# Kernel optimization log

Measured on AMD Instinct MI355X. Metric: run time of the kernel, lower is better.

The kernel has to match this reference:

```python
import jax, jax.numpy as jnp
import numpy as np

DIM = 512
HEADS = 8
EPS = 1e-3  # keras LayerNormalization default epsilon


def setup_inputs() -> dict:
    key = jax.random.key(0)
    ks = jax.random.split(key, 12)
    B, H, W, C = 8, 32, 32, DIM
    s = 0.02
    return {
        "x": jax.random.normal(ks[0], (B, H, W, C), jnp.float32),
        "ln_gamma": jnp.ones((C,), jnp.float32),
        "ln_beta": jnp.zeros((C,), jnp.float32),
        "qkv_d_w": jax.random.normal(ks[1], (C, 3 * C), jnp.float32) * s,
        "qkv_d_b": jnp.zeros((3 * C,), jnp.float32),
        "qkv_s_w": jax.random.normal(ks[2], (C, 3 * C), jnp.float32) * s,
        "qkv_s_b": jnp.zeros((3 * C,), jnp.float32),
        "proj_d_w": jax.random.normal(ks[3], (C, C), jnp.float32) * s,
        "proj_d_b": jnp.zeros((C,), jnp.float32),
        "proj_s_w": jax.random.normal(ks[4], (C, C), jnp.float32) * s,
        "proj_s_b": jnp.zeros((C,), jnp.float32),
        "fusion_weight": jnp.ones((2,), jnp.float32),
    }


def _split_heads(t, B, N):
    # [B, N, C] -> [B, heads, N, head_dim]
    return t.reshape(B, N, HEADS, -1).transpose(0, 2, 1, 3)


def _merge_heads(t, B, N, C):
    # [B, heads, N, head_dim] -> [B, N, C]
    return t.transpose(0, 2, 1, 3).reshape(B, N, C)


def reference(x, ln_gamma, ln_beta, qkv_d_w, qkv_d_b, qkv_s_w, qkv_s_b,
              proj_d_w, proj_d_b, proj_s_w, proj_s_b, fusion_weight):
    B, H, W, C = x.shape
    N = H * W
    scale = (C // HEADS) ** -0.5

    xf = x.reshape(B, N, C)
    mu = jnp.mean(xf, axis=-1, keepdims=True)
    var = jnp.var(xf, axis=-1, keepdims=True)
    xf = (xf - mu) * jax.lax.rsqrt(var + EPS) * ln_gamma + ln_beta

    # dense (softmax) branch
    qkv_d = xf @ qkv_d_w + qkv_d_b
    q_d, k_d, v_d = (
        _split_heads(t, B, N) for t in jnp.split(qkv_d, 3, axis=-1)
    )
    logits_d = jnp.einsum("bhnd,bhmd->bhnm", q_d, k_d) * scale
    out_d = jnp.einsum("bhnm,bhmd->bhnd", jax.nn.softmax(logits_d, axis=-1), v_d)
    out_d = _merge_heads(out_d, B, N, C) @ proj_d_w + proj_d_b

    # sparse (relu^2) branch
    qkv_s = xf @ qkv_s_w + qkv_s_b
    q_s, k_s, v_s = (
        _split_heads(t, B, N) for t in jnp.split(qkv_s, 3, axis=-1)
    )
    rq = jnp.square(jax.nn.relu(q_s))
    rk = jnp.square(jax.nn.relu(k_s))
    logits_s = jnp.einsum("bhnd,bhmd->bhnm", rq, rk) * scale
    out_s = jnp.einsum("bhnm,bhmd->bhnd", logits_s, v_s)
    out_s = _merge_heads(out_s, B, N, C) @ proj_s_w + proj_s_b

    alpha = jax.nn.softmax(fusion_weight)
    out = alpha[0] * out_s + alpha[1] * out_d
    return out.reshape(B, H, W, C)
```

## Files before the change

### kernel.cpp

```cpp
#include <hip/hip_runtime.h>
#include <math.h>

#define M_ROWS   8192
#define CDIM     512
#define QKV_N    1536
#define NTOK     1024
#define HEADS    8
#define HD       64
#define EPS      1e-3f
#define SCALE    0.125f
#define SCL2E    0.18033688011112042f

typedef __attribute__((ext_vector_type(8))) short short8;
typedef __attribute__((ext_vector_type(4))) float f32x4;
typedef unsigned short ushort_t;


__device__ __forceinline__ ushort_t f2bf(float f) {
    union { float f; unsigned int u; } v; v.f = f;
    unsigned int r = v.u + 0x7fffu + ((v.u >> 16) & 1u);
    return (ushort_t)(r >> 16);
}
__device__ __forceinline__ float bf2f(ushort_t u) {
    union { unsigned int u; float f; } v; v.u = ((unsigned int)u) << 16;
    return v.f;
}

__device__ __forceinline__ void stage16(const void* g, void* l) {
    __builtin_amdgcn_global_load_lds(
        (__attribute__((address_space(1))) void*)(g),
        (__attribute__((address_space(3))) void*)(l), 16, 0, 0);
}

__device__ __forceinline__ void get_alpha(const float* __restrict__ fw,
                                          float& a0, float& a1)
{
    const float m  = fmaxf(fw[0], fw[1]);
    const float e0 = __expf(fw[0] - m);
    const float e1 = __expf(fw[1] - m);
    const float inv = 1.0f / (e0 + e1);
    a0 = e0 * inv;
    a1 = e1 * inv;
}


__device__ __forceinline__ void tconv_body(const float* __restrict__ W,
                                           ushort_t* __restrict__ hiT,
                                           ushort_t* __restrict__ loT,
                                           int N, int ors, int coff,
                                           int bk, int bn, int t,
                                           float (*tile)[65])
{
#pragma unroll
    for (int i = 0; i < 4; ++i) {
        const int idx = t + i * 256;
        const int kl = idx >> 4, nl = (idx & 15) * 4;
        const float4 v = *(const float4*)(W + (size_t)(bk + kl) * N + bn + nl);
        tile[kl][nl] = v.x; tile[kl][nl + 1] = v.y;
        tile[kl][nl + 2] = v.z; tile[kl][nl + 3] = v.w;
    }
    __syncthreads();
#pragma unroll
    for (int i = 0; i < 2; ++i) {
        const int idx = t + i * 256;
        const int nl = idx >> 3, kc = (idx & 7) * 8;
        short8 hv, lv;
#pragma unroll
        for (int j = 0; j < 8; ++j) {
            const float f = tile[kc + j][nl];
            const ushort_t h = f2bf(f);
            hv[j] = (short)h;
            lv[j] = (short)f2bf(f - bf2f(h));
        }
        const size_t ob = (size_t)(bn + nl) * ors + coff + bk + kc;
        *(short8*)(hiT + ob) = hv;
        if (loT) *(short8*)(loT + ob) = lv;
    }
}

__global__ __launch_bounds__(256) void prep_kernel(const float* __restrict__ x,
                                                   const float* __restrict__ gamma,
                                                   const float* __restrict__ beta,
                                                   ushort_t* __restrict__ xhi,
                                                   ushort_t* __restrict__ xlo,
                                                   const float* __restrict__ qkv_d_w,
                                                   ushort_t* __restrict__ WdT_hi,
                                                   const float* __restrict__ qkv_s_w,
                                                   ushort_t* __restrict__ WsT_hi,
                                                   ushort_t* __restrict__ WsT_lo,
                                                   const float* __restrict__ proj_s_w,
                                                   const float* __restrict__ proj_d_w,
                                                   ushort_t* __restrict__ WpT_hi,
                                                   ushort_t* __restrict__ WpT_lo,
                                                   const float* __restrict__ bs,
                                                   const float* __restrict__ bd,
                                                   const float* __restrict__ fw,
                                                   float* __restrict__ biasc)
{
    __shared__ float tile[64][65];
    const int t = threadIdx.x;
    const int blk = blockIdx.x;

    if (blk < 2048) {
        const int wv   = t >> 6, lane = t & 63;
        const int row  = blk * 4 + wv;
        const float* xr = x + (size_t)row * CDIM + lane * 8;
        const float4 v0 = *(const float4*)(xr);
        const float4 v1 = *(const float4*)(xr + 4);
        float s  = (v0.x + v0.y) + (v0.z + v0.w) + (v1.x + v1.y) + (v1.z + v1.w);
        float ss = (v0.x * v0.x + v0.y * v0.y) + (v0.z * v0.z + v0.w * v0.w)
                 + (v1.x * v1.x + v1.y * v1.y) + (v1.z * v1.z + v1.w * v1.w);
#pragma unroll
        for (int off = 32; off > 0; off >>= 1) {
            s  += __shfl_xor(s,  off, 64);
            ss += __shfl_xor(ss, off, 64);
        }
        const float mu  = s * (1.0f / CDIM);
        const float var = ss * (1.0f / CDIM) - mu * mu;
        const float rs  = rsqrtf(var + EPS);
        const float4 g0 = *(const float4*)(gamma + lane * 8);
        const float4 g1 = *(const float4*)(gamma + lane * 8 + 4);
        const float4 b0 = *(const float4*)(beta + lane * 8);
        const float4 b1 = *(const float4*)(beta + lane * 8 + 4);
        float o[8];
        o[0] = (v0.x - mu) * rs * g0.x + b0.x;
        o[1] = (v0.y - mu) * rs * g0.y + b0.y;
        o[2] = (v0.z - mu) * rs * g0.z + b0.z;
        o[3] = (v0.w - mu) * rs * g0.w + b0.w;
        o[4] = (v1.x - mu) * rs * g1.x + b1.x;
        o[5] = (v1.y - mu) * rs * g1.y + b1.y;
        o[6] = (v1.z - mu) * rs * g1.z + b1.z;
        o[7] = (v1.w - mu) * rs * g1.w + b1.w;
        short8 hv, lv;
#pragma unroll
        for (int j = 0; j < 8; ++j) {
            const ushort_t h = f2bf(o[j]);
            hv[j] = (short)h;
            lv[j] = (short)f2bf(o[j] - bf2f(h));
        }
        *(short8*)(xhi + (size_t)row * CDIM + lane * 8) = hv;
        *(short8*)(xlo + (size_t)row * CDIM + lane * 8) = lv;
        return;
    }
    int idx = blk - 2048;
    if (idx < 192) {
        tconv_body(qkv_d_w, WdT_hi, nullptr, QKV_N, CDIM, 0,
                   (idx & 7) * 64, (idx >> 3) * 64, t, tile);
        return;
    }
    idx -= 192;
    if (idx < 192) {
        tconv_body(qkv_s_w, WsT_hi, WsT_lo, QKV_N, CDIM, 0,
                   (idx & 7) * 64, (idx >> 3) * 64, t, tile);
        return;
    }
    idx -= 192;
    if (idx < 64) {
        tconv_body(proj_s_w, WpT_hi, WpT_lo, CDIM, 1024, 0,
                   (idx & 7) * 64, (idx >> 3) * 64, t, tile);
        return;
    }
    idx -= 64;
    if (idx < 64) {
        tconv_body(proj_d_w, WpT_hi, nullptr, CDIM, 1024, 512,
                   (idx & 7) * 64, (idx >> 3) * 64, t, tile);
        return;
    }
    float a0, a1;
    get_alpha(fw, a0, a1);
    biasc[t]       = a0 * bs[t]       + a1 * bd[t];
    biasc[t + 256] = a0 * bs[t + 256] + a1 * bd[t + 256];
}


template<int MODE, int OUTBF>
__global__ __launch_bounds__(256) void gemm_bf16_mfma(const ushort_t* __restrict__ Ahi,
                                                      const ushort_t* __restrict__ Alo,
                                                      const ushort_t* __restrict__ Bhi,
                                                      const ushort_t* __restrict__ Blo,
                                                      const float* __restrict__ bias,
                                                      float* __restrict__ C,
                                                      ushort_t* __restrict__ Cb,
                                                      int N, int K)
{
    const int t  = threadIdx.x;
    const int l  = t & 63, w = t >> 6;
    const int wr = w >> 1, wc = w & 1;
    const int lr = l & 15, lg = l >> 4;
    const int bm = blockIdx.x * 128, bn = blockIdx.y * 128;

    __shared__ ushort_t As[MODE ? 2 : 1][128 * 64];
    __shared__ ushort_t Bs[MODE ? 2 : 1][128 * 64];

    f32x4 acc[4][4];
#pragma unroll
    for (int i = 0; i < 4; ++i)
#pragma unroll
        for (int j = 0; j < 4; ++j) acc[i][j] = (f32x4){0.f, 0.f, 0.f, 0.f};

    const int srow8 = t >> 3;
    const int sch   = ((t & 7) ^ ((t >> 3) & 7)) * 8;
    const int lbase = (t >> 6) * 512;

    for (int kt = 0; kt < K; kt += 64) {
        __syncthreads();
#pragma unroll
        for (int i = 0; i < 4; ++i) {
            const int row = srow8 + i * 32;
            const size_t ga = (size_t)(bm + row) * K + kt + sch;
            const size_t gb = (size_t)(bn + row) * K + kt + sch;
            stage16(Ahi + ga, &As[0][i * 2048 + lbase]);
            stage16(Bhi + gb, &Bs[0][i * 2048 + lbase]);
            if (MODE) {
                stage16(Alo + ga, &As[MODE ? 1 : 0][i * 2048 + lbase]);
                stage16(Blo + gb, &Bs[MODE ? 1 : 0][i * 2048 + lbase]);
            }
        }
        __syncthreads();
#pragma unroll
        for (int ks = 0; ks < 2; ++ks) {
            short8 ah[4], bh[4], al[4], bl[4];
#pragma unroll
            for (int mf = 0; mf < 4; ++mf) {
                const int row = wr * 64 + mf * 16 + lr;
                const int cs  = (((ks * 4 + lg) ^ (row & 7)) * 8);
                ah[mf] = *(const short8*)(&As[0][row * 64 + cs]);
                if (MODE) al[mf] = *(const short8*)(&As[MODE ? 1 : 0][row * 64 + cs]);
            }
#pragma unroll
            for (int nf = 0; nf < 4; ++nf) {
                const int row = wc * 64 + nf * 16 + lr;
                const int cs  = (((ks * 4 + lg) ^ (row & 7)) * 8);
                bh[nf] = *(const short8*)(&Bs[0][row * 64 + cs]);
                if (MODE) bl[nf] = *(const short8*)(&Bs[MODE ? 1 : 0][row * 64 + cs]);
            }
#pragma unroll
            for (int mf = 0; mf < 4; ++mf)
#pragma unroll
                for (int nf = 0; nf < 4; ++nf) {
                    acc[mf][nf] = __builtin_amdgcn_mfma_f32_16x16x32_bf16(ah[mf], bh[nf], acc[mf][nf], 0, 0, 0);
                    if (MODE) {
                        acc[mf][nf] = __builtin_amdgcn_mfma_f32_16x16x32_bf16(al[mf], bh[nf], acc[mf][nf], 0, 0, 0);
                        acc[mf][nf] = __builtin_amdgcn_mfma_f32_16x16x32_bf16(ah[mf], bl[nf], acc[mf][nf], 0, 0, 0);
                    }
                }
        }
    }
    float bv[4];
#pragma unroll
    for (int nf = 0; nf < 4; ++nf) bv[nf] = bias[bn + wc * 64 + nf * 16 + lr];
    const float oscl = (OUTBF && bn < 512) ? SCL2E : 1.0f;
#pragma unroll
    for (int mf = 0; mf < 4; ++mf)
#pragma unroll
        for (int r = 0; r < 4; ++r) {
            const int row = bm + wr * 64 + mf * 16 + lg * 4 + r;
            if (OUTBF) {
                ushort_t* cp = Cb + (size_t)row * N + bn + wc * 64;
#pragma unroll
                for (int nf = 0; nf < 4; ++nf)
                    cp[nf * 16 + lr] = f2bf((acc[mf][nf][r] + bv[nf]) * oscl);
            } else {
                float* cp = C + (size_t)row * N + bn + wc * 64;
#pragma unroll
                for (int nf = 0; nf < 4; ++nf)
                    cp[nf * 16 + lr] = acc[mf][nf][r] + bv[nf];
            }
        }
}


__global__ __launch_bounds__(256) void gemm_proj(const ushort_t* __restrict__ Ahi,
                                                 const ushort_t* __restrict__ Alo,
                                                 const ushort_t* __restrict__ Bhi,
                                                 const ushort_t* __restrict__ Blo,
                                                 const float* __restrict__ bias,
                                                 float* __restrict__ C)
{
    const int t  = threadIdx.x;
    const int l  = t & 63, w = t >> 6;
    const int wr = w >> 1, wc = w & 1;
    const int lr = l & 15, lg = l >> 4;
    const int bm = blockIdx.x * 64, bn = blockIdx.y * 128;

    __shared__ ushort_t As[2][64 * 64];
    __shared__ ushort_t Bs[2][128 * 64];

    f32x4 acc[2][4];
#pragma unroll
    for (int i = 0; i < 2; ++i)
#pragma unroll
        for (int j = 0; j < 4; ++j) acc[i][j] = (f32x4){0.f, 0.f, 0.f, 0.f};

    const int srow8 = t >> 3;
    const int sch   = ((t & 7) ^ ((t >> 3) & 7)) * 8;
    const int lbase = (t >> 6) * 512;

    for (int kt = 0; kt < 512; kt += 64) {
        __syncthreads();
#pragma unroll
        for (int i = 0; i < 2; ++i) {
            const size_t ga = (size_t)(bm + srow8 + i * 32) * 1024 + kt + sch;
            stage16(Ahi + ga, &As[0][i * 2048 + lbase]);
            stage16(Alo + ga, &As[1][i * 2048 + lbase]);
        }
#pragma unroll
        for (int i = 0; i < 4; ++i) {
            const size_t gb = (size_t)(bn + srow8 + i * 32) * 1024 + kt + sch;
            stage16(Bhi + gb, &Bs[0][i * 2048 + lbase]);
            stage16(Blo + gb, &Bs[1][i * 2048 + lbase]);
        }
        __syncthreads();
#pragma unroll
        for (int ks = 0; ks < 2; ++ks) {
            short8 ah[2], al[2], bh[4], bl[4];
#pragma unroll
            for (int mf = 0; mf < 2; ++mf) {
                const int row = wr * 32 + mf * 16 + lr;
                const int cs  = (((ks * 4 + lg) ^ (row & 7)) * 8);
                ah[mf] = *(const short8*)(&As[0][row * 64 + cs]);
                al[mf] = *(const short8*)(&As[1][row * 64 + cs]);
            }
#pragma unroll
            for (int nf = 0; nf < 4; ++nf) {
                const int row = wc * 64 + nf * 16 + lr;
                const int cs  = (((ks * 4 + lg) ^ (row & 7)) * 8);
                bh[nf] = *(const short8*)(&Bs[0][row * 64 + cs]);
                bl[nf] = *(const short8*)(&Bs[1][row * 64 + cs]);
            }
#pragma unroll
            for (int mf = 0; mf < 2; ++mf)
#pragma unroll
                for (int nf = 0; nf < 4; ++nf) {
                    acc[mf][nf] = __builtin_amdgcn_mfma_f32_16x16x32_bf16(ah[mf], bh[nf], acc[mf][nf], 0, 0, 0);
                    acc[mf][nf] = __builtin_amdgcn_mfma_f32_16x16x32_bf16(al[mf], bh[nf], acc[mf][nf], 0, 0, 0);
                    acc[mf][nf] = __builtin_amdgcn_mfma_f32_16x16x32_bf16(ah[mf], bl[nf], acc[mf][nf], 0, 0, 0);
                }
        }
    }

    for (int kt = 512; kt < 1024; kt += 64) {
        __syncthreads();
#pragma unroll
        for (int i = 0; i < 2; ++i) {
            const size_t ga = (size_t)(bm + srow8 + i * 32) * 1024 + kt + sch;
            stage16(Ahi + ga, &As[0][i * 2048 + lbase]);
        }
#pragma unroll
        for (int i = 0; i < 4; ++i) {
            const size_t gb = (size_t)(bn + srow8 + i * 32) * 1024 + kt + sch;
            stage16(Bhi + gb, &Bs[0][i * 2048 + lbase]);
        }
        __syncthreads();
#pragma unroll
        for (int ks = 0; ks < 2; ++ks) {
            short8 ah[2], bh[4];
#pragma unroll
            for (int mf = 0; mf < 2; ++mf) {
                const int row = wr * 32 + mf * 16 + lr;
                const int cs  = (((ks * 4 + lg) ^ (row & 7)) * 8);
                ah[mf] = *(const short8*)(&As[0][row * 64 + cs]);
            }
#pragma unroll
            for (int nf = 0; nf < 4; ++nf) {
                const int row = wc * 64 + nf * 16 + lr;
                const int cs  = (((ks * 4 + lg) ^ (row & 7)) * 8);
                bh[nf] = *(const short8*)(&Bs[0][row * 64 + cs]);
            }
#pragma unroll
            for (int mf = 0; mf < 2; ++mf)
#pragma unroll
                for (int nf = 0; nf < 4; ++nf)
                    acc[mf][nf] = __builtin_amdgcn_mfma_f32_16x16x32_bf16(ah[mf], bh[nf], acc[mf][nf], 0, 0, 0);
        }
    }

    float bv[4];
#pragma unroll
    for (int nf = 0; nf < 4; ++nf) bv[nf] = bias[bn + wc * 64 + nf * 16 + lr];
#pragma unroll
    for (int mf = 0; mf < 2; ++mf)
#pragma unroll
        for (int r = 0; r < 4; ++r) {
            const int row = bm + wr * 32 + mf * 16 + lg * 4 + r;
            float* cp = C + (size_t)row * CDIM + bn + wc * 64;
#pragma unroll
            for (int nf = 0; nf < 4; ++nf)
                cp[nf * 16 + lr] = acc[mf][nf][r] + bv[nf];
        }
}


__global__ __launch_bounds__(256) void vt_skv_kernel(const ushort_t* __restrict__ qkvd_bf,
                                                     ushort_t* __restrict__ vtg,
                                                     const float* __restrict__ qkvs,
                                                     float* __restrict__ kvpart)
{
    __shared__ __align__(16) float smem[8704];
    const int t = threadIdx.x;

    if (blockIdx.x < 1024) {
        ushort_t* tile = (ushort_t*)smem;
        const int bh = blockIdx.x & 63, nt = blockIdx.x >> 6;
        const int b  = bh >> 3, h = bh & 7;
        const int row = t >> 2, c16 = (t & 3) * 16;
        const size_t src = (size_t)(b * NTOK + nt * 64 + row) * QKV_N + 2 * CDIM + h * HD + c16;
        *(short8*)(tile + row * 72 + c16)     = *(const short8*)(qkvd_bf + src);
        *(short8*)(tile + row * 72 + c16 + 8) = *(const short8*)(qkvd_bf + src + 8);
        __syncthreads();
        const int d = t >> 2, tc = (t & 3) * 16;
        short8 o0, o1;
#pragma unroll
        for (int i = 0; i < 8; ++i) {
            o0[i] = (short)tile[(tc + i) * 72 + d];
            o1[i] = (short)tile[(tc + 8 + i) * 72 + d];
        }
        const size_t dst = ((size_t)bh * 64 + d) * NTOK + nt * 64 + tc;
        *(short8*)(vtg + dst)     = o0;
        *(short8*)(vtg + dst + 8) = o1;
        return;
    }

    const int bid   = blockIdx.x - 1024;
    const int bh    = bid >> 2;
    const int chunk = bid & 3;
    const int b     = bh >> 3, h = bh & 7;
    const int j     = t >> 2, g = t & 3;
    float* ks = smem;
    float* vs = smem + 64 * 68;
    float4 acc[4];
#pragma unroll
    for (int c4 = 0; c4 < 4; ++c4) acc[c4] = make_float4(0.f, 0.f, 0.f, 0.f);

    const size_t bbase = (size_t)b * NTOK * QKV_N;
    for (int mt = chunk * 4; mt < chunk * 4 + 4; ++mt) {
        __syncthreads();
        {
            const float* ksrc = qkvs + bbase + (size_t)(mt * 64) * QKV_N + CDIM + h * HD;
            const float* vsrc = ksrc + CDIM;
#pragma unroll
            for (int i = 0; i < 4; ++i) {
                const int idx = t + i * 256;
                const int row = idx >> 4, c4 = (idx & 15) * 4;
                *(float4*)(ks + row * 68 + c4) = *(const float4*)(ksrc + (size_t)row * QKV_N + c4);
                *(float4*)(vs + row * 68 + c4) = *(const float4*)(vsrc + (size_t)row * QKV_N + c4);
            }
        }
        __syncthreads();
#pragma unroll 4
        for (int m = 0; m < 64; ++m) {
            const float kkv = ks[m * 68 + j];
            const float rk  = fmaxf(kkv, 0.f);
            const float rk2 = rk * rk;
#pragma unroll
            for (int c4 = 0; c4 < 4; ++c4) {
                const float4 vv = *(const float4*)(vs + m * 68 + g * 16 + c4 * 4);
                acc[c4].x += rk2 * vv.x; acc[c4].y += rk2 * vv.y;
                acc[c4].z += rk2 * vv.z; acc[c4].w += rk2 * vv.w;
            }
        }
    }
#pragma unroll
    for (int c4 = 0; c4 < 4; ++c4) {
        float4 w = acc[c4];
        w.x *= SCALE; w.y *= SCALE; w.z *= SCALE; w.w *= SCALE;
        *(float4*)(kvpart + ((size_t)bid << 12) + j * 64 + g * 16 + c4 * 4) = w;
    }
}


__global__ __launch_bounds__(256) void attn_sout_kernel(const ushort_t* __restrict__ qkvd_bf,
                                                        const ushort_t* __restrict__ vtg,
                                                        const float* __restrict__ qkvs,
                                                        const float* __restrict__ kvpart,
                                                        const float* __restrict__ fw,
                                                        ushort_t* __restrict__ athi,
                                                        ushort_t* __restrict__ atlo)
{
    __shared__ __align__(16) float smem[9216];
    const int t = threadIdx.x;

    if (blockIdx.x < 1024) {
        const int l  = t & 63;
        const int w  = t >> 6;
        const int lr = l & 15;
        const int lg = l >> 4;

        const int blk = blockIdx.x;
        const int xcd = blk & 7;
        const int ixl = blk >> 3;
        const int bh  = ((ixl >> 4) << 3) + xcd;
        const int qt  = ixl & 15;
        const int b   = bh >> 3, h = bh & 7;

        ushort_t* Qs = (ushort_t*)smem;
        ushort_t* Ks = Qs + 64 * 72;
        ushort_t* Vs = Ks + 64 * 72;
        ushort_t* Pq = Vs + 64 * 72;

        const int srow = t >> 2, sc = (t & 3) * 16;
        const size_t kbase = (size_t)(b * NTOK + srow) * QKV_N + CDIM + h * HD + sc;
        const size_t vbase = ((size_t)bh * 64 + srow) * NTOK + sc;

        {
            const size_t src = (size_t)(b * NTOK + qt * 64 + srow) * QKV_N + h * HD + sc;
            *(short8*)(Qs + srow * 72 + sc)     = *(const short8*)(qkvd_bf + src);
            *(short8*)(Qs + srow * 72 + sc + 8) = *(const short8*)(qkvd_bf + src + 8);
        }

        short8 kr0 = *(const short8*)(qkvd_bf + kbase);
        short8 kr1 = *(const short8*)(qkvd_bf + kbase + 8);
        short8 vr0 = *(const short8*)(vtg + vbase);
        short8 vr1 = *(const short8*)(vtg + vbase + 8);

        __syncthreads();

        const short8 bQ0 = *(const short8*)(Qs + (w * 16 + lr) * 72 + lg * 8);
        const short8 bQ1 = *(const short8*)(Qs + (w * 16 + lr) * 72 + 32 + lg * 8);

        f32x4 oacc[4];
#pragma unroll
        for (int i = 0; i < 4; ++i) oacc[i] = (f32x4){0.f, 0.f, 0.f, 0.f};
        float lsum = 0.f;

        for (int kt2 = 0; kt2 < 16; ++kt2) {
            *(short8*)(Ks + srow * 72 + sc)     = kr0;
            *(short8*)(Ks + srow * 72 + sc + 8) = kr1;
            *(short8*)(Vs + srow * 72 + sc)     = vr0;
            *(short8*)(Vs + srow * 72 + sc + 8) = vr1;
            __syncthreads();

            if (kt2 < 15) {
                const size_t ksrc = kbase + (size_t)((kt2 + 1) * 64) * QKV_N;
                const size_t vsrc = vbase + (kt2 + 1) * 64;
                kr0 = *(const short8*)(qkvd_bf + ksrc);
                kr1 = *(const short8*)(qkvd_bf + ksrc + 8);
                vr0 = *(const short8*)(vtg + vsrc);
                vr1 = *(const short8*)(vtg + vsrc + 8);
            }

#pragma unroll
            for (int kb = 0; kb < 4; ++kb) {
                const short8 aK0 = *(const short8*)(Ks + (kb * 16 + lr) * 72 + lg * 8);
                const short8 aK1 = *(const short8*)(Ks + (kb * 16 + lr) * 72 + 32 + lg * 8);
                f32x4 z = {0.f, 0.f, 0.f, 0.f};
                __builtin_amdgcn_s_setprio(1);
                z = __builtin_amdgcn_mfma_f32_16x16x32_bf16(aK0, bQ0, z, 0, 0, 0);
                z = __builtin_amdgcn_mfma_f32_16x16x32_bf16(aK1, bQ1, z, 0, 0, 0);
                __builtin_amdgcn_s_setprio(0);
                const float p0 = exp2f(z[0]);
                const float p1 = exp2f(z[1]);
                const float p2 = exp2f(z[2]);
                const float p3 = exp2f(z[3]);
                lsum += (p0 + p1) + (p2 + p3);
                unsigned int r01, r23;
                asm("v_cvt_pk_bf16_f32 %0, %1, %2" : "=v"(r01) : "v"(p0), "v"(p1));
                asm("v_cvt_pk_bf16_f32 %0, %1, %2" : "=v"(r23) : "v"(p2), "v"(p3));
                uint2 pw; pw.x = r01; pw.y = r23;
                *(uint2*)(Pq + (w * 16 + lr) * 72 + kb * 16 + lg * 4) = pw;
            }

            const short8 bP0 = *(const short8*)(Pq + (w * 16 + lr) * 72 + lg * 8);
            const short8 bP1 = *(const short8*)(Pq + (w * 16 + lr) * 72 + 32 + lg * 8);
            __builtin_amdgcn_s_setprio(1);
#pragma unroll
            for (int nfd = 0; nfd < 4; ++nfd) {
                const short8 aV0 = *(const short8*)(Vs + (nfd * 16 + lr) * 72 + lg * 8);
                const short8 aV1 = *(const short8*)(Vs + (nfd * 16 + lr) * 72 + 32 + lg * 8);
                oacc[nfd] = __builtin_amdgcn_mfma_f32_16x16x32_bf16(aV0, bP0, oacc[nfd], 0, 0, 0);
                oacc[nfd] = __builtin_amdgcn_mfma_f32_16x16x32_bf16(aV1, bP1, oacc[nfd], 0, 0, 0);
            }
            __builtin_amdgcn_s_setprio(0);
            __syncthreads();
        }

        lsum += __shfl_xor(lsum, 16, 64);
        lsum += __shfl_xor(lsum, 32, 64);
        float a0, a1;
        get_alpha(fw, a0, a1);
        const float sc2 = a1 / lsum;
        const size_t orow = ((size_t)(b * NTOK + qt * 64 + w * 16 + lr)) * 1024 + CDIM + h * HD;
#pragma unroll
        for (int nfd = 0; nfd < 4; ++nfd) {
            ushort4 hw;
#pragma unroll
            for (int r = 0; r < 4; ++r)
                ((ushort_t*)&hw)[r] = f2bf(oacc[nfd][r] * sc2);
            *(ushort4*)(athi + orow + nfd * 16 + lg * 4) = hw;
        }
        return;
    }

    const int blk = blockIdx.x - 1024;
    const int qt  = blk & 15;
    const int bh  = blk >> 4;
    const int b   = bh >> 3, h = bh & 7;
    const int r   = t >> 2, g = t & 3;
    float* qs  = smem;
    float* kvs = smem + 64 * 68;
    {
        const float* qsrc = qkvs + (size_t)b * NTOK * QKV_N + (size_t)(qt * 64) * QKV_N + h * HD;
        const float* p0 = kvpart + ((size_t)(bh * 4) << 12);
#pragma unroll
        for (int i = 0; i < 4; ++i) {
            const int idx = t + i * 256;
            const int row = idx >> 4, c4 = (idx & 15) * 4;
            *(float4*)(qs + row * 68 + c4) = *(const float4*)(qsrc + (size_t)row * QKV_N + c4);
            const int o = row * 64 + c4;
            float4 s0 = *(const float4*)(p0 + o);
            const float4 s1 = *(const float4*)(p0 + 4096 + o);
            const float4 s2 = *(const float4*)(p0 + 8192 + o);
            const float4 s3 = *(const float4*)(p0 + 12288 + o);
            s0.x += s1.x + s2.x + s3.x; s0.y += s1.y + s2.y + s3.y;
            s0.z += s1.z + s2.z + s3.z; s0.w += s1.w + s2.w + s3.w;
            *(float4*)(kvs + row * 68 + c4) = s0;
        }
    }
    __syncthreads();
    float4 acc[4];
#pragma unroll
    for (int c4 = 0; c4 < 4; ++c4) acc[c4] = make_float4(0.f, 0.f, 0.f, 0.f);
#pragma unroll 4
    for (int jj = 0; jj < 64; ++jj) {
        const float qv  = qs[r * 68 + jj];
        const float rq  = fmaxf(qv, 0.f);
        const float rq2 = rq * rq;
#pragma unroll
        for (int c4 = 0; c4 < 4; ++c4) {
            const float4 kvv = *(const float4*)(kvs + jj * 68 + g * 16 + c4 * 4);
            acc[c4].x += rq2 * kvv.x; acc[c4].y += rq2 * kvv.y;
            acc[c4].z += rq2 * kvv.z; acc[c4].w += rq2 * kvv.w;
        }
    }
    float a0, a1;
    get_alpha(fw, a0, a1);
    const size_t orow = ((size_t)(b * NTOK + qt * 64 + r)) * 1024 + h * HD;
#pragma unroll
    for (int c4 = 0; c4 < 4; ++c4) {
        float4 w = acc[c4];
        w.x *= a0; w.y *= a0; w.z *= a0; w.w *= a0;
        ushort4 hw, lw;
        hw.x = f2bf(w.x); lw.x = f2bf(w.x - bf2f(hw.x));
        hw.y = f2bf(w.y); lw.y = f2bf(w.y - bf2f(hw.y));
        hw.z = f2bf(w.z); lw.z = f2bf(w.z - bf2f(hw.z));
        hw.w = f2bf(w.w); lw.w = f2bf(w.w - bf2f(hw.w));
        *(ushort4*)(athi + orow + g * 16 + c4 * 4) = hw;
        *(ushort4*)(atlo + orow + g * 16 + c4 * 4) = lw;
    }
}


extern "C" void kernel_launch(void* const* d_in, const int* in_sizes, int n_in,
                              void* d_out, int out_size, void* d_ws, size_t ws_size,
                              hipStream_t stream)
{
    (void)in_sizes; (void)n_in; (void)out_size; (void)ws_size;

    const float* x        = (const float*)d_in[0];
    const float* ln_g     = (const float*)d_in[1];
    const float* ln_b     = (const float*)d_in[2];
    const float* qkv_d_w  = (const float*)d_in[3];
    const float* qkv_d_b  = (const float*)d_in[4];
    const float* qkv_s_w  = (const float*)d_in[5];
    const float* qkv_s_b  = (const float*)d_in[6];
    const float* proj_d_w = (const float*)d_in[7];
    const float* proj_d_b = (const float*)d_in[8];
    const float* proj_s_w = (const float*)d_in[9];
    const float* proj_s_b = (const float*)d_in[10];
    const float* fw       = (const float*)d_in[11];

    float* ws = (float*)d_ws;
    float*    qkvs    = ws;
    float*    kvpart  = ws + (size_t)12582912;
    float*    biasc   = ws + (size_t)13631488;
    ushort_t* qkvd_bf = (ushort_t*)(ws + (size_t)14680064);
    ushort_t* vtg     = (ushort_t*)(ws + (size_t)20971520);
    ushort_t* athi    = (ushort_t*)(ws + (size_t)23068672);
    ushort_t* atlo    = (ushort_t*)(ws + (size_t)27262976);
    ushort_t* xhi     = (ushort_t*)(ws + (size_t)31457280);
    ushort_t* xlo     = (ushort_t*)(ws + (size_t)33554432);
    ushort_t* WdT_hi  = (ushort_t*)(ws + (size_t)35651584);
    ushort_t* WsT_hi  = (ushort_t*)(ws + (size_t)36044800);
    ushort_t* WsT_lo  = (ushort_t*)(ws + (size_t)36438016);
    ushort_t* WpT_hi  = (ushort_t*)(ws + (size_t)36831232);
    ushort_t* WpT_lo  = (ushort_t*)(ws + (size_t)37093376);

    prep_kernel<<<2561, 256, 0, stream>>>(x, ln_g, ln_b, xhi, xlo,
                                          qkv_d_w, WdT_hi,
                                          qkv_s_w, WsT_hi, WsT_lo,
                                          proj_s_w, proj_d_w, WpT_hi, WpT_lo,
                                          proj_s_b, proj_d_b, fw, biasc);

    gemm_bf16_mfma<0, 1><<<dim3(64, 12), 256, 0, stream>>>(xhi, nullptr, WdT_hi, nullptr,
                                                           qkv_d_b, nullptr, qkvd_bf,
                                                           QKV_N, CDIM);
    gemm_bf16_mfma<1, 0><<<dim3(64, 12), 256, 0, stream>>>(xhi, xlo, WsT_hi, WsT_lo,
                                                           qkv_s_b, qkvs, nullptr,
                                                           QKV_N, CDIM);

    vt_skv_kernel<<<1280, 256, 0, stream>>>(qkvd_bf, vtg, qkvs, kvpart);
    attn_sout_kernel<<<2048, 256, 0, stream>>>(qkvd_bf, vtg, qkvs, kvpart, fw, athi, atlo);

    gemm_proj<<<dim3(128, 4), 256, 0, stream>>>(athi, atlo, WpT_hi, WpT_lo,
                                                biasc, (float*)d_out);
}
```

Before: 176.6 us.

## Process two query tiles per attention block to reuse staged K/V tiles

Each dense-attention block now handles 128 query rows (two 64-row halves) instead of 64, so every K/V tile staged in shared memory serves twice as many queries. The dense part of the grid drops from 1024 to 512 blocks, halving global K/V traffic and the staging and barrier overhead per query. In exchange each thread holds twice the accumulators and Q fragments, which raises register pressure and can lower occupancy, and there are fewer blocks to spread across the GPU.

```diff
diff --git a/kernel.cpp b/kernel.cpp
--- a/kernel.cpp
+++ b/kernel.cpp
@@ -480,7 +480,7 @@
     __shared__ __align__(16) float smem[9216];
     const int t = threadIdx.x;
 
-    if (blockIdx.x < 1024) {
+    if (blockIdx.x < 512) {
         const int l  = t & 63;
         const int w  = t >> 6;
         const int lr = l & 15;
@@ -489,8 +489,8 @@
         const int blk = blockIdx.x;
         const int xcd = blk & 7;
         const int ixl = blk >> 3;
-        const int bh  = ((ixl >> 4) << 3) + xcd;
-        const int qt  = ixl & 15;
+        const int bh  = ((ixl >> 3) << 3) + xcd;
+        const int qt  = ixl & 7;
         const int b   = bh >> 3, h = bh & 7;
 
         ushort_t* Qs = (ushort_t*)smem;
@@ -502,10 +502,16 @@
         const size_t kbase = (size_t)(b * NTOK + srow) * QKV_N + CDIM + h * HD + sc;
         const size_t vbase = ((size_t)bh * 64 + srow) * NTOK + sc;
 
-        {
-            const size_t src = (size_t)(b * NTOK + qt * 64 + srow) * QKV_N + h * HD + sc;
+        short8 bQ0[2], bQ1[2];
+#pragma unroll
+        for (int qh = 0; qh < 2; ++qh) {
+            const size_t src = (size_t)(b * NTOK + qt * 128 + qh * 64 + srow) * QKV_N + h * HD + sc;
             *(short8*)(Qs + srow * 72 + sc)     = *(const short8*)(qkvd_bf + src);
             *(short8*)(Qs + srow * 72 + sc + 8) = *(const short8*)(qkvd_bf + src + 8);
+            __syncthreads();
+            bQ0[qh] = *(const short8*)(Qs + (w * 16 + lr) * 72 + lg * 8);
+            bQ1[qh] = *(const short8*)(Qs + (w * 16 + lr) * 72 + 32 + lg * 8);
+            __syncthreads();
         }
 
         short8 kr0 = *(const short8*)(qkvd_bf + kbase);
@@ -513,15 +519,12 @@
         short8 vr0 = *(const short8*)(vtg + vbase);
         short8 vr1 = *(const short8*)(vtg + vbase + 8);
 
-        __syncthreads();
-
-        const short8 bQ0 = *(const short8*)(Qs + (w * 16 + lr) * 72 + lg * 8);
-        const short8 bQ1 = *(const short8*)(Qs + (w * 16 + lr) * 72 + 32 + lg * 8);
-
-        f32x4 oacc[4];
-#pragma unroll
-        for (int i = 0; i < 4; ++i) oacc[i] = (f32x4){0.f, 0.f, 0.f, 0.f};
-        float lsum = 0.f;
+        f32x4 oacc[2][4];
+#pragma unroll
+        for (int qh = 0; qh < 2; ++qh)
+#pragma unroll
+            for (int i = 0; i < 4; ++i) oacc[qh][i] = (f32x4){0.f, 0.f, 0.f, 0.f};
+        float lsum[2] = {0.f, 0.f};
 
         for (int kt2 = 0; kt2 < 16; ++kt2) {
             *(short8*)(Ks + srow * 72 + sc)     = kr0;
@@ -540,58 +543,64 @@
             }
 
 #pragma unroll
-            for (int kb = 0; kb < 4; ++kb) {
-                const short8 aK0 = *(const short8*)(Ks + (kb * 16 + lr) * 72 + lg * 8);
-                const short8 aK1 = *(const short8*)(Ks + (kb * 16 + lr) * 72 + 32 + lg * 8);
-                f32x4 z = {0.f, 0.f, 0.f, 0.f};
+            for (int qh = 0; qh < 2; ++qh) {
+#pragma unroll
+                for (int kb = 0; kb < 4; ++kb) {
+                    const short8 aK0 = *(const short8*)(Ks + (kb * 16 + lr) * 72 + lg * 8);
+                    const short8 aK1 = *(const short8*)(Ks + (kb * 16 + lr) * 72 + 32 + lg * 8);
+                    f32x4 z = {0.f, 0.f, 0.f, 0.f};
+                    __builtin_amdgcn_s_setprio(1);
+                    z = __builtin_amdgcn_mfma_f32_16x16x32_bf16(aK0, bQ0[qh], z, 0, 0, 0);
+                    z = __builtin_amdgcn_mfma_f32_16x16x32_bf16(aK1, bQ1[qh], z, 0, 0, 0);
+                    __builtin_amdgcn_s_setprio(0);
+                    const float p0 = exp2f(z[0]);
+                    const float p1 = exp2f(z[1]);
+                    const float p2 = exp2f(z[2]);
+                    const float p3 = exp2f(z[3]);
+                    lsum[qh] += (p0 + p1) + (p2 + p3);
+                    unsigned int r01, r23;
+                    asm("v_cvt_pk_bf16_f32 %0, %1, %2" : "=v"(r01) : "v"(p0), "v"(p1));
+                    asm("v_cvt_pk_bf16_f32 %0, %1, %2" : "=v"(r23) : "v"(p2), "v"(p3));
+                    uint2 pw; pw.x = r01; pw.y = r23;
+                    *(uint2*)(Pq + (w * 16 + lr) * 72 + kb * 16 + lg * 4) = pw;
+                }
+                const short8 bP0 = *(const short8*)(Pq + (w * 16 + lr) * 72 + lg * 8);
+                const short8 bP1 = *(const short8*)(Pq + (w * 16 + lr) * 72 + 32 + lg * 8);
                 __builtin_amdgcn_s_setprio(1);
-                z = __builtin_amdgcn_mfma_f32_16x16x32_bf16(aK0, bQ0, z, 0, 0, 0);
-                z = __builtin_amdgcn_mfma_f32_16x16x32_bf16(aK1, bQ1, z, 0, 0, 0);
+#pragma unroll
+                for (int nfd = 0; nfd < 4; ++nfd) {
+                    const short8 aV0 = *(const short8*)(Vs + (nfd * 16 + lr) * 72 + lg * 8);
+                    const short8 aV1 = *(const short8*)(Vs + (nfd * 16 + lr) * 72 + 32 + lg * 8);
+                    oacc[qh][nfd] = __builtin_amdgcn_mfma_f32_16x16x32_bf16(aV0, bP0, oacc[qh][nfd], 0, 0, 0);
+                    oacc[qh][nfd] = __builtin_amdgcn_mfma_f32_16x16x32_bf16(aV1, bP1, oacc[qh][nfd], 0, 0, 0);
+                }
                 __builtin_amdgcn_s_setprio(0);
-                const float p0 = exp2f(z[0]);
-                const float p1 = exp2f(z[1]);
-                const float p2 = exp2f(z[2]);
-                const float p3 = exp2f(z[3]);
-                lsum += (p0 + p1) + (p2 + p3);
-                unsigned int r01, r23;
-                asm("v_cvt_pk_bf16_f32 %0, %1, %2" : "=v"(r01) : "v"(p0), "v"(p1));
-                asm("v_cvt_pk_bf16_f32 %0, %1, %2" : "=v"(r23) : "v"(p2), "v"(p3));
-                uint2 pw; pw.x = r01; pw.y = r23;
-                *(uint2*)(Pq + (w * 16 + lr) * 72 + kb * 16 + lg * 4) = pw;
-            }
-
-            const short8 bP0 = *(const short8*)(Pq + (w * 16 + lr) * 72 + lg * 8);
-            const short8 bP1 = *(const short8*)(Pq + (w * 16 + lr) * 72 + 32 + lg * 8);
-            __builtin_amdgcn_s_setprio(1);
-#pragma unroll
-            for (int nfd = 0; nfd < 4; ++nfd) {
-                const short8 aV0 = *(const short8*)(Vs + (nfd * 16 + lr) * 72 + lg * 8);
-                const short8 aV1 = *(const short8*)(Vs + (nfd * 16 + lr) * 72 + 32 + lg * 8);
-                oacc[nfd] = __builtin_amdgcn_mfma_f32_16x16x32_bf16(aV0, bP0, oacc[nfd], 0, 0, 0);
-                oacc[nfd] = __builtin_amdgcn_mfma_f32_16x16x32_bf16(aV1, bP1, oacc[nfd], 0, 0, 0);
-            }
-            __builtin_amdgcn_s_setprio(0);
+            }
             __syncthreads();
         }
 
-        lsum += __shfl_xor(lsum, 16, 64);
-        lsum += __shfl_xor(lsum, 32, 64);
         float a0, a1;
         get_alpha(fw, a0, a1);
-        const float sc2 = a1 / lsum;
-        const size_t orow = ((size_t)(b * NTOK + qt * 64 + w * 16 + lr)) * 1024 + CDIM + h * HD;
-#pragma unroll
-        for (int nfd = 0; nfd < 4; ++nfd) {
-            ushort4 hw;
-#pragma unroll
-            for (int r = 0; r < 4; ++r)
-                ((ushort_t*)&hw)[r] = f2bf(oacc[nfd][r] * sc2);
-            *(ushort4*)(athi + orow + nfd * 16 + lg * 4) = hw;
+#pragma unroll
+        for (int qh = 0; qh < 2; ++qh) {
+            float ls = lsum[qh];
+            ls += __shfl_xor(ls, 16, 64);
+            ls += __shfl_xor(ls, 32, 64);
+            const float sc2 = a1 / ls;
+            const size_t orow = ((size_t)(b * NTOK + qt * 128 + qh * 64 + w * 16 + lr)) * 1024 + CDIM + h * HD;
+#pragma unroll
+            for (int nfd = 0; nfd < 4; ++nfd) {
+                ushort4 hw;
+#pragma unroll
+                for (int r = 0; r < 4; ++r)
+                    ((ushort_t*)&hw)[r] = f2bf(oacc[qh][nfd][r] * sc2);
+                *(ushort4*)(athi + orow + nfd * 16 + lg * 4) = hw;
+            }
         }
         return;
     }
 
-    const int blk = blockIdx.x - 1024;
+    const int blk = blockIdx.x - 512;
     const int qt  = blk & 15;
     const int bh  = blk >> 4;
     const int b   = bh >> 3, h = bh & 7;
@@ -699,7 +708,7 @@
                                                            QKV_N, CDIM);
 
     vt_skv_kernel<<<1280, 256, 0, stream>>>(qkvd_bf, vtg, qkvs, kvpart);
-    attn_sout_kernel<<<2048, 256, 0, stream>>>(qkvd_bf, vtg, qkvs, kvpart, fw, athi, atlo);
+    attn_sout_kernel<<<1536, 256, 0, stream>>>(qkvd_bf, vtg, qkvs, kvpart, fw, athi, atlo);
 
     gemm_proj<<<dim3(128, 4), 256, 0, stream>>>(athi, atlo, WpT_hi, WpT_lo,
                                                 biasc, (float*)d_out);
```

Result: no change. 178.5 us (+1.0%).
